# Kernel optimization log

Hardware: AMD Instinct MI355X
Metric: run time of the kernel (lower is better)

The kernel has to match this reference:

```python
import jax, jax.numpy as jnp
import numpy as np

N_NODES = 50000
N_EDGES = 800000
IN_C, HID_C, OUT_C = 256, 512, 256
DROP_P = 0.5


def _glorot(key, fan_in, fan_out):
    lim = float(np.sqrt(6.0 / (fan_in + fan_out)))
    return jax.random.uniform(key, (fan_in, fan_out), jnp.float32, -lim, lim)


def setup_inputs() -> dict:
    key = jax.random.key(0)
    k_x, k_e, k_w1, k_w2 = jax.random.split(key, 4)
    tensor = jax.random.normal(k_x, (N_NODES, IN_C), dtype=jnp.float32)
    edge_index = jax.random.randint(k_e, (2, N_EDGES), 0, N_NODES, dtype=jnp.int64)
    W1 = _glorot(k_w1, IN_C, HID_C)
    b1 = jnp.zeros((HID_C,), jnp.float32)
    W2 = _glorot(k_w2, HID_C, OUT_C)
    b2 = jnp.zeros((OUT_C,), jnp.float32)
    return {"tensor": tensor, "edge_index": edge_index,
            "W1": W1, "b1": b1, "W2": W2, "b2": b2}


def _gcn_conv(x, W, b, row, col, n_nodes):
    # PyG GCNConv: x' = D^-1/2 (A + I) D^-1/2 (x W) + b
    x = x @ W                                            # [N, F_out]
    # degree over targets including self-loops
    deg = jax.ops.segment_sum(jnp.ones_like(col, dtype=x.dtype), col,
                              num_segments=n_nodes) + 1.0
    dinv = jnp.where(deg > 0, jax.lax.rsqrt(deg), 0.0)   # [N]
    norm = dinv[row] * dinv[col]                         # [E]
    msg = x[row] * norm[:, None]                         # [E, F_out] gather
    out = jax.ops.segment_sum(msg, col, num_segments=n_nodes)  # scatter-add
    out = out + x * (dinv * dinv)[:, None]               # self-loop term
    return out + b


def _dropout(x, key, p=DROP_P):
    keep = jax.random.bernoulli(key, 1.0 - p, x.shape)
    return jnp.where(keep, x / (1.0 - p), 0.0)


def reference(tensor, edge_index, W1, b1, W2, b2):
    row, col = edge_index[0], edge_index[1]
    k1, k2 = jax.random.split(jax.random.key(42))
    x = _gcn_conv(tensor, W1, b1, row, col, N_NODES)
    x = _dropout(jax.nn.relu(x), k1)
    x = _gcn_conv(x, W2, b2, row, col, N_NODES)
    x = _dropout(jax.nn.relu(x), k2)
    return x
```

## Files before the change

kernel.cpp:

```cpp
#include <hip/hip_runtime.h>
#include <stdint.h>


#define N_NODES 50000
#define N_EDGES 800000
#define M_PAD   50048
#define IN_C 256
#define HID_C 512
#define OUT_C 256

typedef __attribute__((ext_vector_type(8))) short bf16x8;
typedef __attribute__((ext_vector_type(4))) float f32x4;

struct U2 { unsigned a, b; };

__host__ __device__ constexpr unsigned rotl32(unsigned x, int d) {
  return (x << d) | (x >> (32 - d));
}

#define TF_ROUND(r) { x0 += x1; x1 = rotl32(x1, (r)); x1 ^= x0; }

__host__ __device__ constexpr U2 threefry2x32(unsigned k0, unsigned k1,
                                              unsigned x0, unsigned x1) {
  unsigned ks2 = k0 ^ k1 ^ 0x1BD11BDAu;
  x0 += k0; x1 += k1;
  TF_ROUND(13) TF_ROUND(15) TF_ROUND(26) TF_ROUND(6)  x0 += k1;  x1 += ks2 + 1u;
  TF_ROUND(17) TF_ROUND(29) TF_ROUND(16) TF_ROUND(24) x0 += ks2; x1 += k0 + 2u;
  TF_ROUND(13) TF_ROUND(15) TF_ROUND(26) TF_ROUND(6)  x0 += k0;  x1 += k1 + 3u;
  TF_ROUND(17) TF_ROUND(29) TF_ROUND(16) TF_ROUND(24) x0 += k1;  x1 += ks2 + 4u;
  TF_ROUND(13) TF_ROUND(15) TF_ROUND(26) TF_ROUND(6)  x0 += ks2; x1 += k0 + 5u;
  return U2{x0, x1};
}

__device__ __forceinline__ ushort f2b(float f) {
  unsigned u = __builtin_bit_cast(unsigned, f);
  unsigned r = (u + 0x7fffu + ((u >> 16) & 1u)) >> 16;
  return (ushort)r;
}
__device__ __forceinline__ float b2f(ushort h) {
  unsigned u = (unsigned)h << 16;
  return __builtin_bit_cast(float, u);
}

__device__ __forceinline__ void gload16(const void* g, void* l) {
  __builtin_amdgcn_global_load_lds(
      (const __attribute__((address_space(1))) void*)g,
      (__attribute__((address_space(3))) void*)l, 16, 0, 0);
}

__global__ void deg_kernel(const int* __restrict__ col, int* __restrict__ cnt, int E) {
  int e = blockIdx.x * 256 + threadIdx.x;
  if (e < E) atomicAdd(&cnt[col[e]], 1);
}

__global__ __launch_bounds__(1024) void scan_local(const int* __restrict__ cnt,
                                                   int* __restrict__ indptr,
                                                   int* __restrict__ chunkSums,
                                                   float* __restrict__ dinv, int n) {
  __shared__ int s[1024];
  int gid = blockIdx.x * 1024 + threadIdx.x;
  int v = (gid < n) ? cnt[gid] : 0;
  if (gid < n) dinv[gid] = rsqrtf((float)v + 1.0f);
  s[threadIdx.x] = v;
  __syncthreads();
#pragma unroll
  for (int off = 1; off < 1024; off <<= 1) {
    int t = (threadIdx.x >= off) ? s[threadIdx.x - off] : 0;
    __syncthreads();
    s[threadIdx.x] += t;
    __syncthreads();
  }
  if (gid < n) indptr[gid] = s[threadIdx.x] - v;
  if (threadIdx.x == 1023) chunkSums[blockIdx.x] = s[1023];
}

__global__ void scan_add(int* __restrict__ indptr, const int* __restrict__ chunkSums,
                         int n, int nChunks, int total) {
  __shared__ int sc[64];
  int gid = blockIdx.x * 256 + threadIdx.x;
  if (threadIdx.x < 64) {
    int lane = threadIdx.x;
    int v = (lane < nChunks) ? chunkSums[lane] : 0;
    int incl = v;
#pragma unroll
    for (int off = 1; off < 64; off <<= 1) {
      int t = __shfl_up(incl, off);
      if (lane >= off) incl += t;
    }
    sc[lane] = incl - v;
  }
  __syncthreads();
  if (gid < n) indptr[gid] += sc[gid >> 10];
  if (gid == 0) indptr[n] = total;
}

__global__ void build_csr(const int* __restrict__ row, const int* __restrict__ col,
                          const int* __restrict__ indptr, int* __restrict__ cursor,
                          const float* __restrict__ dinv,
                          int2* __restrict__ srcW, int E) {
  int e = blockIdx.x * 256 + threadIdx.x;
  if (e < E) {
    int r = row[e];
    int c = col[e];
    int p = indptr[c] + atomicAdd(&cursor[c], 1);
    srcW[p] = make_int2(r << 9, __builtin_bit_cast(int, dinv[r]));
  }
}

__global__ void prep(const float* __restrict__ x, ushort* __restrict__ x16, int n4,
                     unsigned char* __restrict__ mask2,
                     unsigned k20, unsigned k21, int nMaskBytes,
                     const float* __restrict__ W1, const float* __restrict__ W2,
                     ushort* __restrict__ W1T, ushort* __restrict__ W2T,
                     ushort* __restrict__ padDst) {
  int i = blockIdx.x * 256 + threadIdx.x;
  if (i < n4) {
    float4 v = *(const float4*)(x + (size_t)i * 4);
    ushort4 o = make_ushort4(f2b(v.x), f2b(v.y), f2b(v.z), f2b(v.w));
    *(ushort4*)(x16 + (size_t)i * 4) = o;
  }
  if (i < nMaskBytes) {
    unsigned eb = (unsigned)i * 8u;
    unsigned byte = 0;
#pragma unroll
    for (int j = 0; j < 8; ++j) {
      U2 r = threefry2x32(k20, k21, 0u, eb + (unsigned)j);
      byte |= (((r.a ^ r.b) >> 31) & 1u) << j;
    }
    mask2[i] = (unsigned char)byte;
  }
  if (i < IN_C * HID_C) {
    int k = i & (IN_C - 1);
    int n = i >> 8;
    W1T[i] = f2b(W1[(size_t)k * HID_C + n]);
  } else if (i < IN_C * HID_C + HID_C * OUT_C) {
    int j = i - IN_C * HID_C;
    int k = j & (HID_C - 1);
    int n = j >> 9;
    W2T[j] = f2b(W2[(size_t)k * OUT_C + n]);
  }
  if (i < (M_PAD - N_NODES) * IN_C / 8) {
    uint4 z = {0u, 0u, 0u, 0u};
    *(uint4*)(padDst + (size_t)i * 8) = z;
  }
}

#define ROW_ACC(vv, ww)                                                        \
  { a0 += b2f((vv).x) * (ww); a1 += b2f((vv).y) * (ww);                        \
    a2 += b2f((vv).z) * (ww); a3 += b2f((vv).w) * (ww); }

template <bool EPI>
__global__ __launch_bounds__(256, 3) void gather16(const ushort* __restrict__ X,
                                                   const int* __restrict__ indptr,
                                                   const int2* __restrict__ srcW,
                                                   const float* __restrict__ dinv,
                                                   const float* __restrict__ bias,
                                                   void* __restrict__ outp,
                                                   unsigned char* __restrict__ mask1Gen,
                                                   const unsigned char* __restrict__ maskUse,
                                                   unsigned k10, unsigned k11, int N) {
  int wid = (blockIdx.x * 256 + threadIdx.x) >> 6;
  int lane = threadIdx.x & 63;
  if (wid >= N) return;
  int beg = __builtin_amdgcn_readfirstlane(indptr[wid]);
  int end = __builtin_amdgcn_readfirstlane(indptr[wid + 1]);
  float dc = dinv[wid];
  const int f0 = lane * 4;
  const char* Xb = (const char*)X + (unsigned)(lane * 8);
  ushort4 sv = *(const ushort4*)(Xb + ((size_t)wid << 9));
  float a0 = b2f(sv.x) * dc, a1 = b2f(sv.y) * dc,
        a2 = b2f(sv.z) * dc, a3 = b2f(sv.w) * dc;

  int e = beg;
  for (; e + 16 <= end; e += 16) {
    int2 q[16];
#pragma unroll
    for (int j = 0; j < 16; ++j) q[j] = srcW[e + j];
    ushort4 u[16];
#pragma unroll
    for (int j = 0; j < 16; ++j)
      u[j] = *(const ushort4*)(Xb + (unsigned)q[j].x);
#pragma unroll
    for (int j = 0; j < 16; ++j)
      ROW_ACC(u[j], __builtin_bit_cast(float, q[j].y));
  }
  for (; e + 4 <= end; e += 4) {
    int2 q[4];
#pragma unroll
    for (int j = 0; j < 4; ++j) q[j] = srcW[e + j];
    ushort4 u[4];
#pragma unroll
    for (int j = 0; j < 4; ++j)
      u[j] = *(const ushort4*)(Xb + (unsigned)q[j].x);
#pragma unroll
    for (int j = 0; j < 4; ++j)
      ROW_ACC(u[j], __builtin_bit_cast(float, q[j].y));
  }
  for (; e < end; ++e) {
    int2 q = srcW[e];
    ushort4 u = *(const ushort4*)(Xb + (unsigned)q.x);
    ROW_ACC(u, __builtin_bit_cast(float, q.y));
  }
  a0 *= dc; a1 *= dc; a2 *= dc; a3 *= dc;

  if (EPI) {
    float4 bv = *(const float4*)(bias + f0);
    unsigned mk = maskUse[(size_t)wid * 32 + (lane >> 1)];
    int sh = (lane & 1) * 4;
    float v0 = fmaxf(a0 + bv.x, 0.f);
    float v1 = fmaxf(a1 + bv.y, 0.f);
    float v2 = fmaxf(a2 + bv.z, 0.f);
    float v3 = fmaxf(a3 + bv.w, 0.f);
    v0 = ((mk >> (sh + 0)) & 1u) ? 0.f : v0 * 2.0f;
    v1 = ((mk >> (sh + 1)) & 1u) ? 0.f : v1 * 2.0f;
    v2 = ((mk >> (sh + 2)) & 1u) ? 0.f : v2 * 2.0f;
    v3 = ((mk >> (sh + 3)) & 1u) ? 0.f : v3 * 2.0f;
    *(float4*)((float*)outp + (size_t)wid * 256 + f0) = make_float4(v0, v1, v2, v3);
  } else {
    uint2 o;
    o.x = (unsigned)f2b(a0) | ((unsigned)f2b(a1) << 16);
    o.y = (unsigned)f2b(a2) | ((unsigned)f2b(a3) << 16);
    *(uint2*)((ushort*)outp + (size_t)wid * 256 + f0) = o;
    unsigned gl = (unsigned)wid * 64u + (unsigned)lane;
    unsigned eb = gl * 8u;
    unsigned byte = 0;
#pragma unroll
    for (int j = 0; j < 8; ++j) {
      U2 r = threefry2x32(k10, k11, 0u, eb + (unsigned)j);
      byte |= (((r.a ^ r.b) >> 31) & 1u) << j;
    }
    mask1Gen[gl] = (unsigned char)byte;
  }
}

template <bool EPI, int NSTRIP>
__global__ __launch_bounds__(256) void gemm_bf16(const ushort* __restrict__ A,
                                                 const ushort* __restrict__ BT,
                                                 ushort* __restrict__ C,
                                                 int M, int K, int N,
                                                 const float* __restrict__ bias,
                                                 const unsigned char* __restrict__ mask1) {
  __shared__ __align__(16) ushort lds[16384];
  const int nwg = gridDim.x;
  const int orig = blockIdx.x;
  const int q = nwg >> 3, r = nwg & 7;
  const int xcd = orig & 7, loc = orig >> 3;
  const int wg = (xcd < r) ? (xcd * (q + 1) + loc)
                           : (r * (q + 1) + (xcd - r) * q + loc);
  const int bm = (wg / NSTRIP) * 128;
  const int bn = (wg % NSTRIP) * 128;

  const int tid = threadIdx.x;
  const int lane = tid & 63;
  const int wv = tid >> 6;
  const int wr = wv >> 1, wc = wv & 1;

  f32x4 acc[4][4] = {};
  const int xorv = (lane & 7) << 4;

  const int nt = K >> 6;
  for (int t = 0; t < nt; ++t) {
    const int k0 = t << 6;
#pragma unroll
    for (int l = 0; l < 4; ++l) {
      int cid = l * 256 + tid;
      int row = cid >> 3;
      int kcol = ((cid & 7) ^ (row & 7)) * 8;
      gload16(A + (size_t)(bm + row) * K + k0 + kcol, (void*)(lds + cid * 8));
      gload16(BT + (size_t)(bn + row) * K + k0 + kcol, (void*)(lds + 8192 + cid * 8));
    }
    __syncthreads();
    const char* Ab = (const char*)lds;
    const char* Bb = (const char*)(lds + 8192);
#pragma unroll
    for (int ks = 0; ks < 2; ++ks) {
      bf16x8 af[4], bf[4];
      const int kb = (ks * 64 + (lane >> 4) * 16) ^ xorv;
#pragma unroll
      for (int i = 0; i < 4; ++i) {
        int arow = wr * 64 + i * 16 + (lane & 15);
        af[i] = *(const bf16x8*)(Ab + arow * 128 + kb);
        int brow = wc * 64 + i * 16 + (lane & 15);
        bf[i] = *(const bf16x8*)(Bb + brow * 128 + kb);
      }
#pragma unroll
      for (int m = 0; m < 4; ++m)
#pragma unroll
        for (int n = 0; n < 4; ++n)
          acc[m][n] = __builtin_amdgcn_mfma_f32_16x16x32_bf16(bf[n], af[m], acc[m][n], 0, 0, 0);
    }
    __syncthreads();
  }

  const int growb = bm + wr * 64 + (lane & 15);
  const int gcolb = bn + wc * 64 + ((lane >> 4) << 2);
  float4 bias_v[4];
  if (EPI) {
#pragma unroll
    for (int n = 0; n < 4; ++n) bias_v[n] = *(const float4*)(bias + gcolb + n * 16);
  }
#pragma unroll
  for (int m = 0; m < 4; ++m) {
    int grow = growb + m * 16;
    unsigned long long mrow = 0;
    if (EPI)
      mrow = *(const unsigned long long*)(mask1 + (((size_t)grow * N + bn + wc * 64) >> 3));
#pragma unroll
    for (int n = 0; n < 4; ++n) {
      int gcol = gcolb + n * 16;
      float v[4];
#pragma unroll
      for (int r2 = 0; r2 < 4; ++r2) {
        float x = acc[m][n][r2];
        if (EPI) {
          x = fmaxf(x + ((const float*)&bias_v[n])[r2], 0.f);
          int bit = (gcol - (bn + wc * 64)) + r2;
          x = ((mrow >> bit) & 1ull) ? 0.f : x * 2.0f;
        }
        v[r2] = x;
      }
      uint2 o;
      o.x = (unsigned)f2b(v[0]) | ((unsigned)f2b(v[1]) << 16);
      o.y = (unsigned)f2b(v[2]) | ((unsigned)f2b(v[3]) << 16);
      *(uint2*)(C + (size_t)grow * N + gcol) = o;
    }
  }
}

extern "C" void kernel_launch(void* const* d_in, const int* in_sizes, int n_in,
                              void* d_out, int out_size, void* d_ws, size_t ws_size,
                              hipStream_t stream) {
  const float* x  = (const float*)d_in[0];
  const int*   ei = (const int*)d_in[1];
  const float* W1 = (const float*)d_in[2];
  const float* b1 = (const float*)d_in[3];
  const float* W2 = (const float*)d_in[4];
  const float* b2 = (const float*)d_in[5];
  float* out = (float*)d_out;
  (void)in_sizes; (void)n_in; (void)out_size; (void)ws_size;

  const int* row = ei;
  const int* col = ei + N_EDGES;

  char* ws = (char*)d_ws;
  float*  dinv      = (float*) (ws);
  int*    cnt       = (int*)   (ws + (1u << 18));
  int*    cursor    = (int*)   (ws + (2u << 18));
  int*    indptr    = (int*)   (ws + (3u << 18));
  int*    chunkSums = (int*)   (ws + (1u << 20));
  int2*   srcW      = (int2*)  (ws + 2u * (1u << 20));
  ushort* W1T       = (ushort*)(ws + 9u * (1u << 20));
  ushort* W2T       = (ushort*)(ws + 9u * (1u << 20) + (1u << 19));
  unsigned char* mask1 = (unsigned char*)(ws + 10u * (1u << 20));
  unsigned char* mask2 = (unsigned char*)(ws + 14u * (1u << 20));
  ushort* x16       = (ushort*)(ws + 18u * (1u << 20));
  ushort* aggB      = (ushort*)(ws + 44u * (1u << 20));
  ushort* h         = (ushort*)(ws + 70u * (1u << 20));
  ushort* hw2       = (ushort*)(ws + 122u* (1u << 20));

  constexpr U2 K1 = threefry2x32(0u, 42u, 0u, 0u);
  constexpr U2 K2 = threefry2x32(0u, 42u, 0u, 1u);

  (void)hipMemsetAsync(cnt, 0, 2u * (1u << 18), stream);
  deg_kernel<<<(N_EDGES + 255) / 256, 256, 0, stream>>>(col, cnt, N_EDGES);
  const int nChunks = (N_NODES + 1023) / 1024;
  scan_local<<<nChunks, 1024, 0, stream>>>(cnt, indptr, chunkSums, dinv, N_NODES);
  scan_add<<<(N_NODES + 255) / 256, 256, 0, stream>>>(indptr, chunkSums, N_NODES, nChunks, N_EDGES);
  build_csr<<<(N_EDGES + 255) / 256, 256, 0, stream>>>(row, col, indptr, cursor, dinv, srcW, N_EDGES);

  prep<<<(N_NODES * IN_C / 4 + 255) / 256, 256, 0, stream>>>(
      x, x16, N_NODES * IN_C / 4, mask2, K2.a, K2.b, N_NODES * 32,
      W1, W2, W1T, W2T, aggB + (size_t)N_NODES * IN_C);

  gather16<false><<<(N_NODES + 3) / 4, 256, 0, stream>>>(
      x16, indptr, srcW, dinv, nullptr, aggB, mask1, nullptr, K1.a, K1.b, N_NODES);
  gemm_bf16<true, HID_C / 128><<<(M_PAD / 128) * (HID_C / 128), 256, 0, stream>>>(
      aggB, W1T, h, M_PAD, IN_C, HID_C, b1, mask1);

  gemm_bf16<false, OUT_C / 128><<<(M_PAD / 128) * (OUT_C / 128), 256, 0, stream>>>(
      h, W2T, hw2, M_PAD, HID_C, OUT_C, nullptr, nullptr);
  gather16<true><<<(N_NODES + 3) / 4, 256, 0, stream>>>(
      hw2, indptr, srcW, dinv, b2, out, nullptr, mask2, 0u, 0u, N_NODES);
}
```

Before: 318.1 us.

## Split gather features into 32-wide chunks with edge-parallel lanes per wave

Stores the bf16 node features in eight chunk-major planes of 32 features each, written by prep and by the second GEMM epilogue. The gather becomes eight blocks per node group, each wave handling one chunk with 8 edge slots of 8 lanes and a shuffle reduction at the end. The intent is a smaller working set per pass so gathered rows hit in L2, plus more memory parallelism per wave. In exchange, indptr and srcW are read eight times, most lanes sit idle in the epilogue, and the grid is eight times larger.

```diff
diff --git a/kernel.cpp b/kernel.cpp
--- a/kernel.cpp
+++ b/kernel.cpp
@@ -8,6 +8,7 @@
 #define IN_C 256
 #define HID_C 512
 #define OUT_C 256
+#define CH ((size_t)M_PAD * 32)
 
 typedef __attribute__((ext_vector_type(8))) short bf16x8;
 typedef __attribute__((ext_vector_type(4))) float f32x4;
@@ -37,9 +38,16 @@
   unsigned r = (u + 0x7fffu + ((u >> 16) & 1u)) >> 16;
   return (ushort)r;
 }
-__device__ __forceinline__ float b2f(ushort h) {
-  unsigned u = (unsigned)h << 16;
-  return __builtin_bit_cast(float, u);
+__device__ __forceinline__ float b2f_hi(unsigned u) {
+  return __builtin_bit_cast(float, u & 0xffff0000u);
+}
+__device__ __forceinline__ float b2f_lo(unsigned u) {
+  return __builtin_bit_cast(float, u << 16);
+}
+
+__device__ __forceinline__ void acc4(float (&a)[4], uint2 u, float wgt) {
+  a[0] += b2f_lo(u.x) * wgt; a[1] += b2f_hi(u.x) * wgt;
+  a[2] += b2f_lo(u.y) * wgt; a[3] += b2f_hi(u.y) * wgt;
 }
 
 __device__ __forceinline__ void gload16(const void* g, void* l) {
@@ -103,11 +111,11 @@
     int r = row[e];
     int c = col[e];
     int p = indptr[c] + atomicAdd(&cursor[c], 1);
-    srcW[p] = make_int2(r << 9, __builtin_bit_cast(int, dinv[r]));
-  }
-}
-
-__global__ void prep(const float* __restrict__ x, ushort* __restrict__ x16, int n4,
+    srcW[p] = make_int2(r << 6, __builtin_bit_cast(int, dinv[r]));
+  }
+}
+
+__global__ void prep(const float* __restrict__ x, ushort* __restrict__ x16c, int n4,
                      unsigned char* __restrict__ mask2,
                      unsigned k20, unsigned k21, int nMaskBytes,
                      const float* __restrict__ W1, const float* __restrict__ W2,
@@ -115,9 +123,12 @@
                      ushort* __restrict__ padDst) {
   int i = blockIdx.x * 256 + threadIdx.x;
   if (i < n4) {
+    int n = i >> 6;
+    int f = (i & 63) * 4;
+    int c = f >> 5, fi = f & 31;
     float4 v = *(const float4*)(x + (size_t)i * 4);
     ushort4 o = make_ushort4(f2b(v.x), f2b(v.y), f2b(v.z), f2b(v.w));
-    *(ushort4*)(x16 + (size_t)i * 4) = o;
+    *(ushort4*)(x16c + (size_t)c * CH + (size_t)n * 32 + fi) = o;
   }
   if (i < nMaskBytes) {
     unsigned eb = (unsigned)i * 8u;
@@ -145,95 +156,101 @@
   }
 }
 
-#define ROW_ACC(vv, ww)                                                        \
-  { a0 += b2f((vv).x) * (ww); a1 += b2f((vv).y) * (ww);                        \
-    a2 += b2f((vv).z) * (ww); a3 += b2f((vv).w) * (ww); }
-
 template <bool EPI>
-__global__ __launch_bounds__(256, 3) void gather16(const ushort* __restrict__ X,
-                                                   const int* __restrict__ indptr,
-                                                   const int2* __restrict__ srcW,
-                                                   const float* __restrict__ dinv,
-                                                   const float* __restrict__ bias,
-                                                   void* __restrict__ outp,
-                                                   unsigned char* __restrict__ mask1Gen,
-                                                   const unsigned char* __restrict__ maskUse,
-                                                   unsigned k10, unsigned k11, int N) {
-  int wid = (blockIdx.x * 256 + threadIdx.x) >> 6;
-  int lane = threadIdx.x & 63;
-  if (wid >= N) return;
-  int beg = __builtin_amdgcn_readfirstlane(indptr[wid]);
-  int end = __builtin_amdgcn_readfirstlane(indptr[wid + 1]);
-  float dc = dinv[wid];
-  const int f0 = lane * 4;
-  const char* Xb = (const char*)X + (unsigned)(lane * 8);
-  ushort4 sv = *(const ushort4*)(Xb + ((size_t)wid << 9));
-  float a0 = b2f(sv.x) * dc, a1 = b2f(sv.y) * dc,
-        a2 = b2f(sv.z) * dc, a3 = b2f(sv.w) * dc;
-
+__global__ __launch_bounds__(256) void gather_chunk(const ushort* __restrict__ Xc,
+                                                    const int* __restrict__ indptr,
+                                                    const int2* __restrict__ srcW,
+                                                    const float* __restrict__ dinv,
+                                                    const float* __restrict__ bias,
+                                                    void* __restrict__ outp,
+                                                    unsigned char* __restrict__ mask1Gen,
+                                                    const unsigned char* __restrict__ maskUse,
+                                                    unsigned k10, unsigned k11, int N) {
+  const int bid = blockIdx.x;
+  const int c = bid & 7;
+  const int g = bid >> 3;
+  const int wv = threadIdx.x >> 6;
+  const int lane = threadIdx.x & 63;
+  const int n = g * 4 + wv;
+  if (n >= N) return;
+  const int slot = lane >> 3;
+  const int fp = lane & 7;
+  const int beg = __builtin_amdgcn_readfirstlane(indptr[n]);
+  const int end = __builtin_amdgcn_readfirstlane(indptr[n + 1]);
+  const float dc = dinv[n];
+  const char* Xb = (const char*)(Xc + (size_t)c * CH) + fp * 8;
+
+  float a[4] = {};
+  if (slot == 0) {
+    uint2 u = *(const uint2*)(Xb + ((size_t)n << 6));
+    acc4(a, u, dc);
+  }
   int e = beg;
   for (; e + 16 <= end; e += 16) {
-    int2 q[16];
-#pragma unroll
-    for (int j = 0; j < 16; ++j) q[j] = srcW[e + j];
-    ushort4 u[16];
-#pragma unroll
-    for (int j = 0; j < 16; ++j)
-      u[j] = *(const ushort4*)(Xb + (unsigned)q[j].x);
-#pragma unroll
-    for (int j = 0; j < 16; ++j)
-      ROW_ACC(u[j], __builtin_bit_cast(float, q[j].y));
-  }
-  for (; e + 4 <= end; e += 4) {
-    int2 q[4];
-#pragma unroll
-    for (int j = 0; j < 4; ++j) q[j] = srcW[e + j];
-    ushort4 u[4];
-#pragma unroll
-    for (int j = 0; j < 4; ++j)
-      u[j] = *(const ushort4*)(Xb + (unsigned)q[j].x);
-#pragma unroll
-    for (int j = 0; j < 4; ++j)
-      ROW_ACC(u[j], __builtin_bit_cast(float, q[j].y));
-  }
-  for (; e < end; ++e) {
-    int2 q = srcW[e];
-    ushort4 u = *(const ushort4*)(Xb + (unsigned)q.x);
-    ROW_ACC(u, __builtin_bit_cast(float, q.y));
-  }
-  a0 *= dc; a1 *= dc; a2 *= dc; a3 *= dc;
+    int2 qa = srcW[e + slot];
+    int2 qb = srcW[e + 8 + slot];
+    uint2 ua = *(const uint2*)(Xb + (unsigned)qa.x);
+    uint2 ub = *(const uint2*)(Xb + (unsigned)qb.x);
+    acc4(a, ua, __builtin_bit_cast(float, qa.y));
+    acc4(a, ub, __builtin_bit_cast(float, qb.y));
+  }
+  if (e + 8 <= end) {
+    int2 q = srcW[e + slot];
+    uint2 u = *(const uint2*)(Xb + (unsigned)q.x);
+    acc4(a, u, __builtin_bit_cast(float, q.y));
+    e += 8;
+  }
+  if (e + slot < end) {
+    int2 q = srcW[e + slot];
+    uint2 u = *(const uint2*)(Xb + (unsigned)q.x);
+    acc4(a, u, __builtin_bit_cast(float, q.y));
+  }
+#pragma unroll
+  for (int j = 0; j < 4; ++j) {
+    a[j] += __shfl_xor(a[j], 8);
+    a[j] += __shfl_xor(a[j], 16);
+    a[j] += __shfl_xor(a[j], 32);
+    a[j] *= dc;
+  }
 
   if (EPI) {
-    float4 bv = *(const float4*)(bias + f0);
-    unsigned mk = maskUse[(size_t)wid * 32 + (lane >> 1)];
-    int sh = (lane & 1) * 4;
-    float v0 = fmaxf(a0 + bv.x, 0.f);
-    float v1 = fmaxf(a1 + bv.y, 0.f);
-    float v2 = fmaxf(a2 + bv.z, 0.f);
-    float v3 = fmaxf(a3 + bv.w, 0.f);
-    v0 = ((mk >> (sh + 0)) & 1u) ? 0.f : v0 * 2.0f;
-    v1 = ((mk >> (sh + 1)) & 1u) ? 0.f : v1 * 2.0f;
-    v2 = ((mk >> (sh + 2)) & 1u) ? 0.f : v2 * 2.0f;
-    v3 = ((mk >> (sh + 3)) & 1u) ? 0.f : v3 * 2.0f;
-    *(float4*)((float*)outp + (size_t)wid * 256 + f0) = make_float4(v0, v1, v2, v3);
+    if (slot == 0) {
+      int f = c * 32 + fp * 4;
+      float4 bv = *(const float4*)(bias + f);
+      unsigned mk = maskUse[(size_t)n * 32 + c * 4 + (fp >> 1)];
+      int sh = (fp & 1) * 4;
+      float v0 = fmaxf(a[0] + bv.x, 0.f);
+      float v1 = fmaxf(a[1] + bv.y, 0.f);
+      float v2 = fmaxf(a[2] + bv.z, 0.f);
+      float v3 = fmaxf(a[3] + bv.w, 0.f);
+      v0 = ((mk >> (sh + 0)) & 1u) ? 0.f : v0 * 2.0f;
+      v1 = ((mk >> (sh + 1)) & 1u) ? 0.f : v1 * 2.0f;
+      v2 = ((mk >> (sh + 2)) & 1u) ? 0.f : v2 * 2.0f;
+      v3 = ((mk >> (sh + 3)) & 1u) ? 0.f : v3 * 2.0f;
+      *(float4*)((float*)outp + (size_t)n * 256 + f) = make_float4(v0, v1, v2, v3);
+    }
   } else {
-    uint2 o;
-    o.x = (unsigned)f2b(a0) | ((unsigned)f2b(a1) << 16);
-    o.y = (unsigned)f2b(a2) | ((unsigned)f2b(a3) << 16);
-    *(uint2*)((ushort*)outp + (size_t)wid * 256 + f0) = o;
-    unsigned gl = (unsigned)wid * 64u + (unsigned)lane;
-    unsigned eb = gl * 8u;
-    unsigned byte = 0;
-#pragma unroll
-    for (int j = 0; j < 8; ++j) {
-      U2 r = threefry2x32(k10, k11, 0u, eb + (unsigned)j);
-      byte |= (((r.a ^ r.b) >> 31) & 1u) << j;
-    }
-    mask1Gen[gl] = (unsigned char)byte;
-  }
-}
-
-template <bool EPI, int NSTRIP>
+    if (slot == 0) {
+      uint2 o;
+      o.x = (unsigned)f2b(a[0]) | ((unsigned)f2b(a[1]) << 16);
+      o.y = (unsigned)f2b(a[2]) | ((unsigned)f2b(a[3]) << 16);
+      *(uint2*)((ushort*)outp + (size_t)n * 256 + c * 32 + fp * 4) = o;
+    }
+    if ((g & 7) == c) {
+      unsigned gl = (unsigned)n * 64u + (unsigned)lane;
+      unsigned eb = gl * 8u;
+      unsigned byte = 0;
+#pragma unroll
+      for (int j = 0; j < 8; ++j) {
+        U2 r = threefry2x32(k10, k11, 0u, eb + (unsigned)j);
+        byte |= (((r.a ^ r.b) >> 31) & 1u) << j;
+      }
+      mask1Gen[gl] = (unsigned char)byte;
+    }
+  }
+}
+
+template <bool EPI, int NSTRIP, bool CHUNKOUT>
 __global__ __launch_bounds__(256) void gemm_bf16(const ushort* __restrict__ A,
                                                  const ushort* __restrict__ BT,
                                                  ushort* __restrict__ C,
@@ -322,7 +339,12 @@
       uint2 o;
       o.x = (unsigned)f2b(v[0]) | ((unsigned)f2b(v[1]) << 16);
       o.y = (unsigned)f2b(v[2]) | ((unsigned)f2b(v[3]) << 16);
-      *(uint2*)(C + (size_t)grow * N + gcol) = o;
+      if (CHUNKOUT) {
+        int cch = gcol >> 5, fi = gcol & 31;
+        *(uint2*)(C + (size_t)cch * CH + (size_t)grow * 32 + fi) = o;
+      } else {
+        *(uint2*)(C + (size_t)grow * N + gcol) = o;
+      }
     }
   }
 }
@@ -353,10 +375,10 @@
   ushort* W2T       = (ushort*)(ws + 9u * (1u << 20) + (1u << 19));
   unsigned char* mask1 = (unsigned char*)(ws + 10u * (1u << 20));
   unsigned char* mask2 = (unsigned char*)(ws + 14u * (1u << 20));
-  ushort* x16       = (ushort*)(ws + 18u * (1u << 20));
+  ushort* x16c      = (ushort*)(ws + 18u * (1u << 20));
   ushort* aggB      = (ushort*)(ws + 44u * (1u << 20));
   ushort* h         = (ushort*)(ws + 70u * (1u << 20));
-  ushort* hw2       = (ushort*)(ws + 122u* (1u << 20));
+  ushort* hw2c      = (ushort*)(ws + 122u* (1u << 20));
 
   constexpr U2 K1 = threefry2x32(0u, 42u, 0u, 0u);
   constexpr U2 K2 = threefry2x32(0u, 42u, 0u, 1u);
@@ -369,16 +391,18 @@
   build_csr<<<(N_EDGES + 255) / 256, 256, 0, stream>>>(row, col, indptr, cursor, dinv, srcW, N_EDGES);
 
   prep<<<(N_NODES * IN_C / 4 + 255) / 256, 256, 0, stream>>>(
-      x, x16, N_NODES * IN_C / 4, mask2, K2.a, K2.b, N_NODES * 32,
+      x, x16c, N_NODES * IN_C / 4, mask2, K2.a, K2.b, N_NODES * 32,
       W1, W2, W1T, W2T, aggB + (size_t)N_NODES * IN_C);
 
-  gather16<false><<<(N_NODES + 3) / 4, 256, 0, stream>>>(
-      x16, indptr, srcW, dinv, nullptr, aggB, mask1, nullptr, K1.a, K1.b, N_NODES);
-  gemm_bf16<true, HID_C / 128><<<(M_PAD / 128) * (HID_C / 128), 256, 0, stream>>>(
+  const int gatherGrid = 8 * ((N_NODES + 3) / 4);
+
+  gather_chunk<false><<<gatherGrid, 256, 0, stream>>>(
+      x16c, indptr, srcW, dinv, nullptr, aggB, mask1, nullptr, K1.a, K1.b, N_NODES);
+  gemm_bf16<true, HID_C / 128, false><<<(M_PAD / 128) * (HID_C / 128), 256, 0, stream>>>(
       aggB, W1T, h, M_PAD, IN_C, HID_C, b1, mask1);
 
-  gemm_bf16<false, OUT_C / 128><<<(M_PAD / 128) * (OUT_C / 128), 256, 0, stream>>>(
-      h, W2T, hw2, M_PAD, HID_C, OUT_C, nullptr, nullptr);
-  gather16<true><<<(N_NODES + 3) / 4, 256, 0, stream>>>(
-      hw2, indptr, srcW, dinv, b2, out, nullptr, mask2, 0u, 0u, N_NODES);
-}
+  gemm_bf16<false, OUT_C / 128, true><<<(M_PAD / 128) * (OUT_C / 128), 256, 0, stream>>>(
+      h, W2T, hw2c, M_PAD, HID_C, OUT_C, nullptr, nullptr);
+  gather_chunk<true><<<gatherGrid, 256, 0, stream>>>(
+      hw2c, indptr, srcW, dinv, b2, out, nullptr, mask2, 0u, 0u, N_NODES);
+}
```

Result: slower. 603.0 us (+89.5%).

## Stage gathered neighbor rows through LDS with 16-byte direct global-to-LDS loads

Applied to the files above, without the earlier changes.

The SpMM gather kernel is rewritten so that each wave loads up to 16 neighbor rows straight into shared memory. It uses global_load_lds with 16-byte lanes, two rows per instruction, then waits and reads the rows back from LDS to accumulate. This replaces 8-byte per-lane register gathers with fewer, wider memory instructions. The bf16 unpack is also simplified by masking and shifting packed 32-bit words. The cost is 32KB of LDS per block, a full vmcnt(0) stall per batch with no overlap between load and compute, and the drop of the 3-waves occupancy hint.

```diff
diff --git a/kernel.cpp b/kernel.cpp
--- a/kernel.cpp
+++ b/kernel.cpp
@@ -37,9 +37,16 @@
   unsigned r = (u + 0x7fffu + ((u >> 16) & 1u)) >> 16;
   return (ushort)r;
 }
-__device__ __forceinline__ float b2f(ushort h) {
-  unsigned u = (unsigned)h << 16;
-  return __builtin_bit_cast(float, u);
+__device__ __forceinline__ float b2f_hi(unsigned u) {
+  return __builtin_bit_cast(float, u & 0xffff0000u);
+}
+__device__ __forceinline__ float b2f_lo(unsigned u) {
+  return __builtin_bit_cast(float, u << 16);
+}
+
+__device__ __forceinline__ void acc4u(float (&a)[4], uint2 u, float wgt) {
+  a[0] += b2f_lo(u.x) * wgt; a[1] += b2f_hi(u.x) * wgt;
+  a[2] += b2f_lo(u.y) * wgt; a[3] += b2f_hi(u.y) * wgt;
 }
 
 __device__ __forceinline__ void gload16(const void* g, void* l) {
@@ -145,72 +152,72 @@
   }
 }
 
-#define ROW_ACC(vv, ww)                                                        \
-  { a0 += b2f((vv).x) * (ww); a1 += b2f((vv).y) * (ww);                        \
-    a2 += b2f((vv).z) * (ww); a3 += b2f((vv).w) * (ww); }
-
 template <bool EPI>
-__global__ __launch_bounds__(256, 3) void gather16(const ushort* __restrict__ X,
-                                                   const int* __restrict__ indptr,
-                                                   const int2* __restrict__ srcW,
-                                                   const float* __restrict__ dinv,
-                                                   const float* __restrict__ bias,
-                                                   void* __restrict__ outp,
-                                                   unsigned char* __restrict__ mask1Gen,
-                                                   const unsigned char* __restrict__ maskUse,
-                                                   unsigned k10, unsigned k11, int N) {
-  int wid = (blockIdx.x * 256 + threadIdx.x) >> 6;
-  int lane = threadIdx.x & 63;
+__global__ __launch_bounds__(256) void gather_lds(const ushort* __restrict__ X,
+                                                  const int* __restrict__ indptr,
+                                                  const int2* __restrict__ srcW,
+                                                  const float* __restrict__ dinv,
+                                                  const float* __restrict__ bias,
+                                                  void* __restrict__ outp,
+                                                  unsigned char* __restrict__ mask1Gen,
+                                                  const unsigned char* __restrict__ maskUse,
+                                                  unsigned k10, unsigned k11, int N) {
+  __shared__ __align__(16) ushort sbuf[4 * 16 * 256];
+  const int wv = threadIdx.x >> 6;
+  const int lane = threadIdx.x & 63;
+  const int wid = (blockIdx.x * 256 + threadIdx.x) >> 6;
   if (wid >= N) return;
-  int beg = __builtin_amdgcn_readfirstlane(indptr[wid]);
-  int end = __builtin_amdgcn_readfirstlane(indptr[wid + 1]);
-  float dc = dinv[wid];
+  ushort* sw = sbuf + wv * 4096;
+
+  const int beg = __builtin_amdgcn_readfirstlane(indptr[wid]);
+  const int end = __builtin_amdgcn_readfirstlane(indptr[wid + 1]);
+  const float dc = dinv[wid];
+  const char* Xb = (const char*)X;
+
+  float a[4] = {};
+  {
+    uint2 u = *(const uint2*)(Xb + ((size_t)wid << 9) + lane * 8);
+    acc4u(a, u, dc);
+  }
+
+  int e = beg;
+  while (e < end) {
+    int cnt = end - e;
+    if (cnt > 16) cnt = 16;
+    const int npair = (cnt + 1) >> 1;
+#pragma unroll
+    for (int j = 0; j < 8; ++j) {
+      if (j < npair) {
+        int i1 = 2 * j + (lane >> 5);
+        if (i1 >= cnt) i1 = 2 * j;
+        int2 q = srcW[e + i1];
+        gload16(Xb + (unsigned)q.x + (lane & 31) * 16, (void*)(sw + j * 512));
+      }
+    }
+    asm volatile("s_waitcnt vmcnt(0)" ::: "memory");
+    __builtin_amdgcn_sched_barrier(0);
+#pragma unroll
+    for (int i = 0; i < 16; ++i) {
+      if (i < cnt) {
+        float w = __builtin_bit_cast(float, srcW[e + i].y);
+        uint2 u = *(const uint2*)(sw + i * 256 + lane * 4);
+        acc4u(a, u, w);
+      }
+    }
+    e += cnt;
+  }
+#pragma unroll
+  for (int j = 0; j < 4; ++j) a[j] *= dc;
+
   const int f0 = lane * 4;
-  const char* Xb = (const char*)X + (unsigned)(lane * 8);
-  ushort4 sv = *(const ushort4*)(Xb + ((size_t)wid << 9));
-  float a0 = b2f(sv.x) * dc, a1 = b2f(sv.y) * dc,
-        a2 = b2f(sv.z) * dc, a3 = b2f(sv.w) * dc;
-
-  int e = beg;
-  for (; e + 16 <= end; e += 16) {
-    int2 q[16];
-#pragma unroll
-    for (int j = 0; j < 16; ++j) q[j] = srcW[e + j];
-    ushort4 u[16];
-#pragma unroll
-    for (int j = 0; j < 16; ++j)
-      u[j] = *(const ushort4*)(Xb + (unsigned)q[j].x);
-#pragma unroll
-    for (int j = 0; j < 16; ++j)
-      ROW_ACC(u[j], __builtin_bit_cast(float, q[j].y));
-  }
-  for (; e + 4 <= end; e += 4) {
-    int2 q[4];
-#pragma unroll
-    for (int j = 0; j < 4; ++j) q[j] = srcW[e + j];
-    ushort4 u[4];
-#pragma unroll
-    for (int j = 0; j < 4; ++j)
-      u[j] = *(const ushort4*)(Xb + (unsigned)q[j].x);
-#pragma unroll
-    for (int j = 0; j < 4; ++j)
-      ROW_ACC(u[j], __builtin_bit_cast(float, q[j].y));
-  }
-  for (; e < end; ++e) {
-    int2 q = srcW[e];
-    ushort4 u = *(const ushort4*)(Xb + (unsigned)q.x);
-    ROW_ACC(u, __builtin_bit_cast(float, q.y));
-  }
-  a0 *= dc; a1 *= dc; a2 *= dc; a3 *= dc;
-
   if (EPI) {
     float4 bv = *(const float4*)(bias + f0);
     unsigned mk = maskUse[(size_t)wid * 32 + (lane >> 1)];
     int sh = (lane & 1) * 4;
-    float v0 = fmaxf(a0 + bv.x, 0.f);
-    float v1 = fmaxf(a1 + bv.y, 0.f);
-    float v2 = fmaxf(a2 + bv.z, 0.f);
-    float v3 = fmaxf(a3 + bv.w, 0.f);
+    float v0 = fmaxf(a[0] + bv.x, 0.f);
+    float v1 = fmaxf(a[1] + bv.y, 0.f);
+    float v2 = fmaxf(a[2] + bv.z, 0.f);
+    float v3 = fmaxf(a[3] + bv.w, 0.f);
     v0 = ((mk >> (sh + 0)) & 1u) ? 0.f : v0 * 2.0f;
     v1 = ((mk >> (sh + 1)) & 1u) ? 0.f : v1 * 2.0f;
     v2 = ((mk >> (sh + 2)) & 1u) ? 0.f : v2 * 2.0f;
@@ -218,8 +225,8 @@
     *(float4*)((float*)outp + (size_t)wid * 256 + f0) = make_float4(v0, v1, v2, v3);
   } else {
     uint2 o;
-    o.x = (unsigned)f2b(a0) | ((unsigned)f2b(a1) << 16);
-    o.y = (unsigned)f2b(a2) | ((unsigned)f2b(a3) << 16);
+    o.x = (unsigned)f2b(a[0]) | ((unsigned)f2b(a[1]) << 16);
+    o.y = (unsigned)f2b(a[2]) | ((unsigned)f2b(a[3]) << 16);
     *(uint2*)((ushort*)outp + (size_t)wid * 256 + f0) = o;
     unsigned gl = (unsigned)wid * 64u + (unsigned)lane;
     unsigned eb = gl * 8u;
@@ -372,13 +379,13 @@
       x, x16, N_NODES * IN_C / 4, mask2, K2.a, K2.b, N_NODES * 32,
       W1, W2, W1T, W2T, aggB + (size_t)N_NODES * IN_C);
 
-  gather16<false><<<(N_NODES + 3) / 4, 256, 0, stream>>>(
+  gather_lds<false><<<(N_NODES + 3) / 4, 256, 0, stream>>>(
       x16, indptr, srcW, dinv, nullptr, aggB, mask1, nullptr, K1.a, K1.b, N_NODES);
   gemm_bf16<true, HID_C / 128><<<(M_PAD / 128) * (HID_C / 128), 256, 0, stream>>>(
       aggB, W1T, h, M_PAD, IN_C, HID_C, b1, mask1);
 
   gemm_bf16<false, OUT_C / 128><<<(M_PAD / 128) * (OUT_C / 128), 256, 0, stream>>>(
       h, W2T, hw2, M_PAD, HID_C, OUT_C, nullptr, nullptr);
-  gather16<true><<<(N_NODES + 3) / 4, 256, 0, stream>>>(
+  gather_lds<true><<<(N_NODES + 3) / 4, 256, 0, stream>>>(
       hw2, indptr, srcW, dinv, b2, out, nullptr, mask2, 0u, 0u, N_NODES);
 }
```

After: 395.4 us. +24.3%, slower.
